# Optimization experiments

Measured on AMD Instinct MI355X. Metric: run time of the kernel, lower is better.

The kernel has to match this reference:

```python
import jax, jax.numpy as jnp
import numpy as np

N, C, H = 4096, 1024, 16
HD = C // H            # 64
DR = HD // 8           # 8 rope freqs per spatial axis


def setup_inputs() -> dict:
    key = jax.random.key(0)
    k1, k2, k3, k4, k5, k6 = jax.random.split(key, 6)
    x = jax.random.normal(k1, (N, C), dtype=jnp.float32)
    coords = jax.random.randint(k2, (N, 5), 0, 64, dtype=jnp.int32)  # [batch, t, h, w, z]
    w_qkv = jax.random.normal(k3, (3 * C, C), dtype=jnp.float32) / np.sqrt(C)
    w_out = jax.random.normal(k4, (C, C), dtype=jnp.float32) / np.sqrt(C)
    gamma_q = jnp.ones((H, HD), dtype=jnp.float32)
    gamma_k = jnp.ones((H, HD), dtype=jnp.float32)
    return {"x": x, "coords": coords, "w_qkv": w_qkv, "w_out": w_out,
            "gamma_q": gamma_q, "gamma_k": gamma_k}


def _rms_norm(t, gamma):
    # F.normalize(dim=-1) * gamma * sqrt(head_dim), computed in fp32
    t = t.astype(jnp.float32)
    nrm = jnp.linalg.norm(t, axis=-1, keepdims=True)
    return t / jnp.maximum(nrm, 1e-12) * gamma * np.float32(np.sqrt(HD))


def _rope_angles(coords):
    # freqs = 1/10000^(arange(DR)/HD); angles per axis (t,h,w,z), concat -> [N, 4*DR] = [N, HD/2]
    freqs = 1.0 / (10000.0 ** (jnp.arange(DR, dtype=jnp.float32) / HD))
    pos = coords[:, 1:].astype(jnp.float32)  # [N,4]
    ang = pos[:, :, None] * freqs[None, None, :]  # [N,4,DR]
    return ang.reshape(ang.shape[0], -1)  # [N, HD/2]


def _apply_rope(t, cos, sin):
    # t: [N,H,HD]; pairs (2i, 2i+1) rotated by angle[i]
    t2 = t.astype(jnp.float32).reshape(t.shape[0], t.shape[1], -1, 2)
    re = t2[..., 0] * cos - t2[..., 1] * sin
    im = t2[..., 0] * sin + t2[..., 1] * cos
    return jnp.stack([re, im], axis=-1).reshape(t.shape)


def reference(x, coords, w_qkv, w_out, gamma_q, gamma_k):
    n = x.shape[0]
    qkv = (x @ w_qkv.T).reshape(n, 3, H, HD)
    q, k, v = qkv[:, 0], qkv[:, 1], qkv[:, 2]  # [N,H,HD]
    q = _rms_norm(q, gamma_q)
    k = _rms_norm(k, gamma_k)
    ang = _rope_angles(coords)              # [N, HD/2]
    cos = jnp.cos(ang)[:, None, :]          # [N,1,HD/2] (broadcast over heads)
    sin = jnp.sin(ang)[:, None, :]
    q = _apply_rope(q, cos, sin)
    k = _apply_rope(k, cos, sin)
    scale = np.float32(1.0 / np.sqrt(HD))
    scores = jnp.einsum('nhd,mhd->hnm', q, k) * scale  # [H,N,N]
    attn = jax.nn.softmax(scores, axis=-1)
    out = jnp.einsum('hnm,mhd->nhd', attn, v).reshape(n, C)
    return out @ w_out.T
```

## Files before the change

kernel.cpp:

```cpp
#include <hip/hip_runtime.h>
#include <hip/hip_bf16.h>

typedef _Float16 half8 __attribute__((ext_vector_type(8)));
typedef _Float16 half4v __attribute__((ext_vector_type(4)));
typedef _Float16 half2 __attribute__((ext_vector_type(2)));
typedef float f32x4 __attribute__((ext_vector_type(4)));

constexpr int NT = 4096;
constexpr int CH = 1024;
constexpr int NH = 16;
constexpr int HD = 64;
constexpr int C3 = 3072;

#if __has_builtin(__builtin_amdgcn_exp2f)
#define EXP2(x) __builtin_amdgcn_exp2f(x)
#else
#define EXP2(x) exp2f(x)
#endif

#define GLOAD_LDS16(gp, lp) __builtin_amdgcn_global_load_lds( \
    (const __attribute__((address_space(1))) void*)(gp),      \
    (__attribute__((address_space(3))) void*)(lp), 16, 0, 0)

#define WAITCNT3 do { asm volatile("s_waitcnt vmcnt(3)" ::: "memory"); \
                      __builtin_amdgcn_sched_barrier(0); } while (0)
#define WAITCNT4 do { asm volatile("s_waitcnt vmcnt(4)" ::: "memory"); \
                      __builtin_amdgcn_sched_barrier(0); } while (0)
#define WAITCNT0 do { asm volatile("s_waitcnt vmcnt(0)" ::: "memory"); \
                      __builtin_amdgcn_sched_barrier(0); } while (0)

static __device__ inline half2 pk_f16(float a, float b) {
  auto r = __builtin_amdgcn_cvt_pkrtz(a, b);
  return *(half2*)&r;
}

__global__ __launch_bounds__(256) void cvt3_kernel(const float* __restrict__ a, int na4,
                                                   const float* __restrict__ b, int nb4,
                                                   const float* __restrict__ c, int nc4,
                                                   _Float16* __restrict__ oa,
                                                   _Float16* __restrict__ ob,
                                                   _Float16* __restrict__ oc) {
  int i = blockIdx.x * 256 + threadIdx.x;
  const float* src; _Float16* dst; int j = i;
  if (i < na4) { src = a; dst = oa; }
  else if (i < na4 + nb4) { src = b; dst = ob; j = i - na4; }
  else if (i < na4 + nb4 + nc4) { src = c; dst = oc; j = i - na4 - nb4; }
  else return;
  float4 v = ((const float4*)src)[j];
  half4v h;
  h[0] = (_Float16)v.x; h[1] = (_Float16)v.y; h[2] = (_Float16)v.z; h[3] = (_Float16)v.w;
  ((half4v*)dst)[j] = h;
}

__global__ __launch_bounds__(256) void rope_tab_kernel(const int* __restrict__ coords,
                                                       float2* __restrict__ csn) {
  int idx = blockIdx.x * 256 + threadIdx.x;
  int n = idx >> 5, j = idx & 31;
  float ang = (float)coords[n * 5 + 1 + (j >> 3)] * __expf(-(float)(j & 7) * 0.14391157f);
  csn[idx] = make_float2(cosf(ang), sinf(ang));
}

__global__ __launch_bounds__(512, 4) void gemm_qkv(const _Float16* __restrict__ A,
                                                   const _Float16* __restrict__ Bt,
                                                   const float2* __restrict__ csn,
                                                   const float* __restrict__ gq,
                                                   const float* __restrict__ gk,
                                                   _Float16* __restrict__ Qh,
                                                   _Float16* __restrict__ KF,
                                                   _Float16* __restrict__ VF) {
  __shared__ __align__(16) char smem[73728];
  auto As = (_Float16(*)[128][32])smem;
  auto Bs = (_Float16(*)[256][32])(smem + 16384);
  const int K = CH;
  const int tid = threadIdx.x;
  const int lane = tid & 63, w = tid >> 6;
  const int l15 = lane & 15, l4 = lane >> 4;
  int nwg = gridDim.x, cpx = nwg >> 3;
  int wg = (blockIdx.x & 7) * cpx + (blockIdx.x >> 3);
  const int nbx = NT / 128;
  const int bm = wg % nbx, bn = wg / nbx;
  const int m0 = bm * 128, n0 = bn * 256;
  const int wr = w >> 2, wc = w & 3;
  const int arow = w * 16 + (lane >> 2);
  const int acol = (lane & 3) * 8;
  const int rb = w * 32;
  const int rl = lane >> 2;
  const int cb = (lane & 3) * 8;
  f32x4 acc[4][4] = {};
  auto stage = [&](int k0, int buf) {
    GLOAD_LDS16(A  + (size_t)(m0 + arow) * K + k0 + acol,       &As[buf][w * 16][0]);
    GLOAD_LDS16(Bt + (size_t)(n0 + rb + rl) * K + k0 + cb,      &Bs[buf][rb][0]);
    GLOAD_LDS16(Bt + (size_t)(n0 + rb + 16 + rl) * K + k0 + cb, &Bs[buf][rb + 16][0]);
  };
  auto compute = [&](int buf) {
    half8 af[4], bf[4];
#pragma unroll
    for (int mt = 0; mt < 4; ++mt) af[mt] = *(half8*)&As[buf][wr * 64 + mt * 16 + l15][l4 * 8];
#pragma unroll
    for (int nt = 0; nt < 4; ++nt) bf[nt] = *(half8*)&Bs[buf][wc * 64 + nt * 16 + l15][l4 * 8];
    __builtin_amdgcn_s_setprio(1);
#pragma unroll
    for (int mt = 0; mt < 4; ++mt)
#pragma unroll
      for (int nt = 0; nt < 4; ++nt)
        acc[mt][nt] = __builtin_amdgcn_mfma_f32_16x16x32_f16(af[mt], bf[nt], acc[mt][nt], 0, 0, 0);
    __builtin_amdgcn_s_setprio(0);
  };
  stage(0, 0);
  stage(32, 1);
  for (int k0 = 0; k0 < K - 32; k0 += 32) {
    int buf = (k0 >> 5) & 1;
    WAITCNT3;
    __builtin_amdgcn_s_barrier();
    compute(buf);
    __builtin_amdgcn_s_barrier();
    if (k0 + 64 < K) stage(k0 + 64, buf);
  }
  WAITCNT0;
  __builtin_amdgcn_s_barrier();
  compute(((K - 32) >> 5) & 1);
  __builtin_amdgcn_s_barrier();
  const int gc0 = n0 + wc * 64;
  const int sec = gc0 >> 10;
  const int h   = (gc0 & 1023) >> 6;
  const int K0  = m0 + wr * 64;
  _Float16* Lw = (_Float16*)(smem + w * 9216);
  if (sec < 2) {
    const float* gm = (sec == 0) ? gq : gk;
    float gmm[4];
#pragma unroll
    for (int nt = 0; nt < 4; ++nt) gmm[nt] = gm[h * 64 + nt * 16 + l15];
    const float qsc = (sec == 0) ? 0.18033688f : 1.0f;
#pragma unroll
    for (int mt = 0; mt < 4; ++mt)
#pragma unroll
      for (int r = 0; r < 4; ++r) {
        float ss = 0.f;
#pragma unroll
        for (int nt = 0; nt < 4; ++nt) ss += acc[mt][nt][r] * acc[mt][nt][r];
        ss += __shfl_xor(ss, 1); ss += __shfl_xor(ss, 2);
        ss += __shfl_xor(ss, 4); ss += __shfl_xor(ss, 8);
        float sc = 8.0f / fmaxf(sqrtf(ss), 1e-12f);
        int row = mt * 16 + l4 * 4 + r;
        int n = K0 + row;
#pragma unroll
        for (int nt = 0; nt < 4; ++nt) {
          float v = acc[mt][nt][r] * sc * gmm[nt];
          float2 cz = csn[n * 32 + nt * 8 + (l15 >> 1)];
          float p = __shfl_xor(v, 1);
          float o = ((l15 & 1) == 0) ? (v * cz.x - p * cz.y) : (p * cz.y + v * cz.x);
          Lw[row * 72 + nt * 16 + l15] = (_Float16)(o * qsc);
        }
      }
  } else {
#pragma unroll
    for (int mt = 0; mt < 4; ++mt)
#pragma unroll
      for (int r = 0; r < 4; ++r) {
        int row = mt * 16 + l4 * 4 + r;
#pragma unroll
        for (int nt = 0; nt < 4; ++nt)
          Lw[row * 72 + nt * 16 + l15] = (_Float16)acc[mt][nt][r];
      }
  }
  const int kb = K0 >> 6;
  if (sec == 0) {
#pragma unroll
    for (int i = 0; i < 8; ++i) {
      int row = i * 8 + (lane >> 3), col = (lane & 7) * 8;
      half8 vv = *(half8*)&Lw[row * 72 + col];
      *(half8*)(Qh + ((size_t)h * NT + K0 + row) * 64 + col) = vv;
    }
  } else if (sec == 1) {
    _Float16* base = KF + (size_t)h * NT * HD + (size_t)kb * 4096;
#pragma unroll
    for (int i = 0; i < 8; ++i) {
      int t = i >> 1, kk = i & 1;
      int i15 = lane & 15, ll4 = lane >> 4;
      int m = ((t >> 1) << 5) | ((i15 >> 2) << 3) | ((t & 1) << 2) | (i15 & 3);
      half8 vv = *(half8*)&Lw[m * 72 + kk * 32 + ll4 * 8];
      *(half8*)(base + (size_t)(((t * 2 + kk) * 64 + ll4 * 16 + i15) * 8)) = vv;
    }
  } else {
    _Float16* base = VF + (size_t)h * NT * HD + (size_t)kb * 4096;
#pragma unroll
    for (int i = 0; i < 8; ++i) {
      int t = i >> 1, kk = i & 1;
      int l15v = lane & 15, l4v = lane >> 4;
      half8 vv;
#pragma unroll
      for (int jj = 0; jj < 8; ++jj)
        vv[jj] = Lw[(kk * 32 + l4v * 8 + jj) * 72 + t * 16 + l15v];
      *(half8*)(base + (size_t)(((t * 2 + kk) * 64 + l4v * 16 + l15v) * 8)) = vv;
    }
  }
}

template <typename OutT>
__global__ __launch_bounds__(256) void gemm_bt(const _Float16* __restrict__ A,
                                               const _Float16* __restrict__ Bt,
                                               OutT* __restrict__ Cc,
                                               int M, int Nn, int K, int nbx) {
  __shared__ _Float16 As[2][128][32];
  __shared__ _Float16 Bs[2][128][32];
  const int tid = threadIdx.x;
  const int lane = tid & 63, w = tid >> 6;
  const int l15 = lane & 15, l4 = lane >> 4;
  int nwg = gridDim.x, cpx = nwg >> 3;
  int wg = (blockIdx.x & 7) * cpx + (blockIdx.x >> 3);
  const int m0 = (wg % nbx) * 128, n0 = (wg / nbx) * 128;
  const int wr = w >> 1, wc = w & 1;
  const int rb = w * 32;
  const int rl = lane >> 2;
  const int cb = (lane & 3) * 8;
  f32x4 acc[4][4] = {};
  auto stage = [&](int k0, int buf) {
    GLOAD_LDS16(A  + (size_t)(m0 + rb + rl) * K + k0 + cb,      &As[buf][rb][0]);
    GLOAD_LDS16(A  + (size_t)(m0 + rb + 16 + rl) * K + k0 + cb, &As[buf][rb + 16][0]);
    GLOAD_LDS16(Bt + (size_t)(n0 + rb + rl) * K + k0 + cb,      &Bs[buf][rb][0]);
    GLOAD_LDS16(Bt + (size_t)(n0 + rb + 16 + rl) * K + k0 + cb, &Bs[buf][rb + 16][0]);
  };
  auto compute = [&](int buf) {
    half8 af[4], bf[4];
#pragma unroll
    for (int mt = 0; mt < 4; ++mt) af[mt] = *(half8*)&As[buf][wr * 64 + mt * 16 + l15][l4 * 8];
#pragma unroll
    for (int nt = 0; nt < 4; ++nt) bf[nt] = *(half8*)&Bs[buf][wc * 64 + nt * 16 + l15][l4 * 8];
    __builtin_amdgcn_s_setprio(1);
#pragma unroll
    for (int mt = 0; mt < 4; ++mt)
#pragma unroll
      for (int nt = 0; nt < 4; ++nt)
        acc[mt][nt] = __builtin_amdgcn_mfma_f32_16x16x32_f16(af[mt], bf[nt], acc[mt][nt], 0, 0, 0);
    __builtin_amdgcn_s_setprio(0);
  };
  stage(0, 0);
  stage(32, 1);
  for (int k0 = 0; k0 < K - 32; k0 += 32) {
    int buf = (k0 >> 5) & 1;
    WAITCNT4;
    __builtin_amdgcn_s_barrier();
    compute(buf);
    __builtin_amdgcn_s_barrier();
    if (k0 + 64 < K) stage(k0 + 64, buf);
  }
  WAITCNT0;
  __builtin_amdgcn_s_barrier();
  compute(((K - 32) >> 5) & 1);
#pragma unroll
  for (int mt = 0; mt < 4; ++mt)
#pragma unroll
    for (int nt = 0; nt < 4; ++nt)
#pragma unroll
      for (int r = 0; r < 4; ++r) {
        int row = m0 + wr * 64 + mt * 16 + l4 * 4 + r;
        int col = n0 + wc * 64 + nt * 16 + l15;
        Cc[(size_t)row * Nn + col] = (OutT)acc[mt][nt][r];
      }
}

__global__ __launch_bounds__(256, 2) void attn_kernel(const _Float16* __restrict__ Qh,
                                                      const _Float16* __restrict__ KF,
                                                      const _Float16* __restrict__ VF,
                                                      _Float16* __restrict__ Oh) {
  __shared__ _Float16 KB[4096];
  __shared__ _Float16 VB[4096];
  const int tid = threadIdx.x, lane = tid & 63, w = tid >> 6;
  const int l15 = lane & 15, l4 = lane >> 4;
  int bid = blockIdx.x;
  int s = bid >> 3;
  int h = (bid & 7) * 2 + (s >> 5);
  int n0 = (s & 31) * 128;
  half8 qf[2][2];
#pragma unroll
  for (int qb = 0; qb < 2; ++qb)
#pragma unroll
    for (int kk = 0; kk < 2; ++kk)
      qf[qb][kk] = *(const half8*)(Qh + ((size_t)h * NT + n0 + w * 32 + qb * 16 + l15) * HD + kk * 32 + l4 * 8);
  f32x4 acc[2][4] = {};
  f32x4 acc5[2] = {};
  half8 of1 = {};
  if (l15 == 0) {
#pragma unroll
    for (int jq = 0; jq < 8; ++jq) of1[jq] = (_Float16)1.0f;
  }
  const _Float16* KFh = KF + (size_t)h * NT * HD + w * 512 + lane * 8;
  const _Float16* VFh = VF + (size_t)h * NT * HD + w * 512 + lane * 8;
  union U { half8 v; half2 p[4]; };
  for (int kb = 0; kb < 64; ++kb) {
    __syncthreads();
    {
      size_t g0 = (size_t)kb * 4096;
      GLOAD_LDS16(KFh + g0,        &KB[w * 512]);
      GLOAD_LDS16(KFh + g0 + 2048, &KB[2048 + w * 512]);
      GLOAD_LDS16(VFh + g0,        &VB[w * 512]);
      GLOAD_LDS16(VFh + g0 + 2048, &VB[2048 + w * 512]);
    }
    __syncthreads();
    f32x4 sv[2][4] = {};
    __builtin_amdgcn_s_setprio(1);
#pragma unroll
    for (int t = 0; t < 4; ++t)
#pragma unroll
      for (int kk = 0; kk < 2; ++kk) {
        half8 kf = *(half8*)&KB[(t * 2 + kk) * 512 + lane * 8];
        sv[0][t] = __builtin_amdgcn_mfma_f32_16x16x32_f16(kf, qf[0][kk], sv[0][t], 0, 0, 0);
        sv[1][t] = __builtin_amdgcn_mfma_f32_16x16x32_f16(kf, qf[1][kk], sv[1][t], 0, 0, 0);
      }
    __builtin_amdgcn_s_setprio(0);
    U u[2][2];
#pragma unroll
    for (int qb = 0; qb < 2; ++qb) {
      float e[4][4];
#pragma unroll
      for (int t = 0; t < 4; ++t)
#pragma unroll
        for (int r = 0; r < 4; ++r) e[t][r] = EXP2(sv[qb][t][r]);
      u[qb][0].p[0] = pk_f16(e[0][0], e[0][1]); u[qb][0].p[1] = pk_f16(e[0][2], e[0][3]);
      u[qb][0].p[2] = pk_f16(e[1][0], e[1][1]); u[qb][0].p[3] = pk_f16(e[1][2], e[1][3]);
      u[qb][1].p[0] = pk_f16(e[2][0], e[2][1]); u[qb][1].p[1] = pk_f16(e[2][2], e[2][3]);
      u[qb][1].p[2] = pk_f16(e[3][0], e[3][1]); u[qb][1].p[3] = pk_f16(e[3][2], e[3][3]);
    }
    __builtin_amdgcn_s_setprio(1);
#pragma unroll
    for (int t = 0; t < 4; ++t)
#pragma unroll
      for (int kk = 0; kk < 2; ++kk) {
        half8 vf = *(half8*)&VB[(t * 2 + kk) * 512 + lane * 8];
        acc[0][t] = __builtin_amdgcn_mfma_f32_16x16x32_f16(u[0][kk].v, vf, acc[0][t], 0, 0, 0);
        acc[1][t] = __builtin_amdgcn_mfma_f32_16x16x32_f16(u[1][kk].v, vf, acc[1][t], 0, 0, 0);
      }
    acc5[0] = __builtin_amdgcn_mfma_f32_16x16x32_f16(u[0][0].v, of1, acc5[0], 0, 0, 0);
    acc5[0] = __builtin_amdgcn_mfma_f32_16x16x32_f16(u[0][1].v, of1, acc5[0], 0, 0, 0);
    acc5[1] = __builtin_amdgcn_mfma_f32_16x16x32_f16(u[1][0].v, of1, acc5[1], 0, 0, 0);
    acc5[1] = __builtin_amdgcn_mfma_f32_16x16x32_f16(u[1][1].v, of1, acc5[1], 0, 0, 0);
    __builtin_amdgcn_s_setprio(0);
  }
#pragma unroll
  for (int qb = 0; qb < 2; ++qb) {
    float linv[4];
#pragma unroll
    for (int r = 0; r < 4; ++r) linv[r] = 1.0f / __shfl(acc5[qb][r], lane & 48);
#pragma unroll
    for (int t = 0; t < 4; ++t)
#pragma unroll
      for (int r = 0; r < 4; ++r) {
        int row = n0 + w * 32 + qb * 16 + l4 * 4 + r;
        Oh[(size_t)row * CH + h * HD + t * 16 + l15] = (_Float16)(acc[qb][t][r] * linv[r]);
      }
  }
}

extern "C" void kernel_launch(void* const* d_in, const int* in_sizes, int n_in,
                              void* d_out, int out_size, void* d_ws, size_t ws_size,
                              hipStream_t stream) {
  const float* x      = (const float*)d_in[0];
  const int*   coords = (const int*)d_in[1];
  const float* w_qkv  = (const float*)d_in[2];
  const float* w_out  = (const float*)d_in[3];
  const float* gq     = (const float*)d_in[4];
  const float* gk     = (const float*)d_in[5];
  float* out = (float*)d_out;

  char* ws = (char*)d_ws;
  size_t off = 0;
  auto alloc = [&](size_t bytes) { char* p = ws + off; off += bytes; return p; };
  _Float16* xh   = (_Float16*)alloc((size_t)NT * CH * 2);
  _Float16* wqh  = (_Float16*)alloc((size_t)C3 * CH * 2);
  _Float16* woh  = (_Float16*)alloc((size_t)CH * CH * 2);
  float2*   csn  = (float2*)alloc((size_t)NT * 32 * 8);
  _Float16* Qh   = (_Float16*)alloc((size_t)NT * CH * 2);
  _Float16* KFh  = (_Float16*)alloc((size_t)NT * CH * 2);
  _Float16* VFh  = (_Float16*)alloc((size_t)NT * CH * 2);
  _Float16* Oh   = (_Float16*)alloc((size_t)NT * CH * 2);
  if (off > ws_size) return;

  int na4 = NT * CH / 4, nb4 = C3 * CH / 4, nc4 = CH * CH / 4;
  cvt3_kernel<<<(na4 + nb4 + nc4) / 256, 256, 0, stream>>>(x, na4, w_qkv, nb4, w_out, nc4,
                                                           xh, wqh, woh);
  rope_tab_kernel<<<NT * 32 / 256, 256, 0, stream>>>(coords, csn);
  gemm_qkv<<<(NT / 128) * (C3 / 256), 512, 0, stream>>>(xh, wqh, csn, gq, gk, Qh, KFh, VFh);
  attn_kernel<<<NH * (NT / 128), 256, 0, stream>>>(Qh, KFh, VFh, Oh);
  gemm_bt<float><<<(NT / 128) * (CH / 128), 256, 0, stream>>>(Oh, woh, out, NT, CH, CH, NT / 128);
}
```

Measured before the change: 154.4 us.

## Replace ones-MFMA row sums with VALU sums and load two KV tiles per barrier

The softmax denominator used to be computed with extra MFMAs against a ones vector. It is now accumulated in fp32 on the vector ALU from the exponentials and reduced across lanes with shuffles at the end. The main loop also fetches two 64-key K/V tiles per iteration into doubled LDS buffers, which halves the number of barrier pairs. This removes four MFMAs per tile and some synchronisation, at the cost of more VALU adds and more LDS use per block, which may lower occupancy.

```diff
diff --git a/kernel.cpp b/kernel.cpp
--- a/kernel.cpp
+++ b/kernel.cpp
@@ -263,8 +263,8 @@
                                                       const _Float16* __restrict__ KF,
                                                       const _Float16* __restrict__ VF,
                                                       _Float16* __restrict__ Oh) {
-  __shared__ _Float16 KB[4096];
-  __shared__ _Float16 VB[4096];
+  __shared__ _Float16 KB[2][4096];
+  __shared__ _Float16 VB[2][4096];
   const int tid = threadIdx.x, lane = tid & 63, w = tid >> 6;
   const int l15 = lane & 15, l4 = lane >> 4;
   int bid = blockIdx.x;
@@ -278,69 +278,77 @@
     for (int kk = 0; kk < 2; ++kk)
       qf[qb][kk] = *(const half8*)(Qh + ((size_t)h * NT + n0 + w * 32 + qb * 16 + l15) * HD + kk * 32 + l4 * 8);
   f32x4 acc[2][4] = {};
-  f32x4 acc5[2] = {};
-  half8 of1 = {};
-  if (l15 == 0) {
-#pragma unroll
-    for (int jq = 0; jq < 8; ++jq) of1[jq] = (_Float16)1.0f;
-  }
+  float ls[2] = {0.f, 0.f};
   const _Float16* KFh = KF + (size_t)h * NT * HD + w * 512 + lane * 8;
   const _Float16* VFh = VF + (size_t)h * NT * HD + w * 512 + lane * 8;
   union U { half8 v; half2 p[4]; };
-  for (int kb = 0; kb < 64; ++kb) {
+  for (int kb = 0; kb < 64; kb += 2) {
     __syncthreads();
     {
       size_t g0 = (size_t)kb * 4096;
-      GLOAD_LDS16(KFh + g0,        &KB[w * 512]);
-      GLOAD_LDS16(KFh + g0 + 2048, &KB[2048 + w * 512]);
-      GLOAD_LDS16(VFh + g0,        &VB[w * 512]);
-      GLOAD_LDS16(VFh + g0 + 2048, &VB[2048 + w * 512]);
+      GLOAD_LDS16(KFh + g0,        &KB[0][w * 512]);
+      GLOAD_LDS16(KFh + g0 + 2048, &KB[0][2048 + w * 512]);
+      GLOAD_LDS16(VFh + g0,        &VB[0][w * 512]);
+      GLOAD_LDS16(VFh + g0 + 2048, &VB[0][2048 + w * 512]);
+      GLOAD_LDS16(KFh + g0 + 4096, &KB[1][w * 512]);
+      GLOAD_LDS16(KFh + g0 + 6144, &KB[1][2048 + w * 512]);
+      GLOAD_LDS16(VFh + g0 + 4096, &VB[1][w * 512]);
+      GLOAD_LDS16(VFh + g0 + 6144, &VB[1][2048 + w * 512]);
     }
     __syncthreads();
-    f32x4 sv[2][4] = {};
-    __builtin_amdgcn_s_setprio(1);
-#pragma unroll
-    for (int t = 0; t < 4; ++t)
-#pragma unroll
-      for (int kk = 0; kk < 2; ++kk) {
-        half8 kf = *(half8*)&KB[(t * 2 + kk) * 512 + lane * 8];
-        sv[0][t] = __builtin_amdgcn_mfma_f32_16x16x32_f16(kf, qf[0][kk], sv[0][t], 0, 0, 0);
-        sv[1][t] = __builtin_amdgcn_mfma_f32_16x16x32_f16(kf, qf[1][kk], sv[1][t], 0, 0, 0);
-      }
-    __builtin_amdgcn_s_setprio(0);
-    U u[2][2];
-#pragma unroll
-    for (int qb = 0; qb < 2; ++qb) {
-      float e[4][4];
+#pragma unroll
+    for (int sub = 0; sub < 2; ++sub) {
+      f32x4 sv[2][4] = {};
+      __builtin_amdgcn_s_setprio(1);
 #pragma unroll
       for (int t = 0; t < 4; ++t)
 #pragma unroll
-        for (int r = 0; r < 4; ++r) e[t][r] = EXP2(sv[qb][t][r]);
-      u[qb][0].p[0] = pk_f16(e[0][0], e[0][1]); u[qb][0].p[1] = pk_f16(e[0][2], e[0][3]);
-      u[qb][0].p[2] = pk_f16(e[1][0], e[1][1]); u[qb][0].p[3] = pk_f16(e[1][2], e[1][3]);
-      u[qb][1].p[0] = pk_f16(e[2][0], e[2][1]); u[qb][1].p[1] = pk_f16(e[2][2], e[2][3]);
-      u[qb][1].p[2] = pk_f16(e[3][0], e[3][1]); u[qb][1].p[3] = pk_f16(e[3][2], e[3][3]);
-    }
-    __builtin_amdgcn_s_setprio(1);
-#pragma unroll
-    for (int t = 0; t < 4; ++t)
-#pragma unroll
-      for (int kk = 0; kk < 2; ++kk) {
-        half8 vf = *(half8*)&VB[(t * 2 + kk) * 512 + lane * 8];
-        acc[0][t] = __builtin_amdgcn_mfma_f32_16x16x32_f16(u[0][kk].v, vf, acc[0][t], 0, 0, 0);
-        acc[1][t] = __builtin_amdgcn_mfma_f32_16x16x32_f16(u[1][kk].v, vf, acc[1][t], 0, 0, 0);
-      }
-    acc5[0] = __builtin_amdgcn_mfma_f32_16x16x32_f16(u[0][0].v, of1, acc5[0], 0, 0, 0);
-    acc5[0] = __builtin_amdgcn_mfma_f32_16x16x32_f16(u[0][1].v, of1, acc5[0], 0, 0, 0);
-    acc5[1] = __builtin_amdgcn_mfma_f32_16x16x32_f16(u[1][0].v, of1, acc5[1], 0, 0, 0);
-    acc5[1] = __builtin_amdgcn_mfma_f32_16x16x32_f16(u[1][1].v, of1, acc5[1], 0, 0, 0);
-    __builtin_amdgcn_s_setprio(0);
+        for (int kk = 0; kk < 2; ++kk) {
+          half8 kf = *(half8*)&KB[sub][(t * 2 + kk) * 512 + lane * 8];
+          sv[0][t] = __builtin_amdgcn_mfma_f32_16x16x32_f16(kf, qf[0][kk], sv[0][t], 0, 0, 0);
+          sv[1][t] = __builtin_amdgcn_mfma_f32_16x16x32_f16(kf, qf[1][kk], sv[1][t], 0, 0, 0);
+        }
+      __builtin_amdgcn_s_setprio(0);
+      U u[2][2];
+#pragma unroll
+      for (int qb = 0; qb < 2; ++qb) {
+        float e[4][4];
+#pragma unroll
+        for (int t = 0; t < 4; ++t)
+#pragma unroll
+          for (int r = 0; r < 4; ++r) e[t][r] = EXP2(sv[qb][t][r]);
+        float s0 = (e[0][0] + e[0][1]) + (e[0][2] + e[0][3]);
+        float s1 = (e[1][0] + e[1][1]) + (e[1][2] + e[1][3]);
+        float s2 = (e[2][0] + e[2][1]) + (e[2][2] + e[2][3]);
+        float s3 = (e[3][0] + e[3][1]) + (e[3][2] + e[3][3]);
+        ls[qb] += (s0 + s1) + (s2 + s3);
+        u[qb][0].p[0] = pk_f16(e[0][0], e[0][1]); u[qb][0].p[1] = pk_f16(e[0][2], e[0][3]);
+        u[qb][0].p[2] = pk_f16(e[1][0], e[1][1]); u[qb][0].p[3] = pk_f16(e[1][2], e[1][3]);
+        u[qb][1].p[0] = pk_f16(e[2][0], e[2][1]); u[qb][1].p[1] = pk_f16(e[2][2], e[2][3]);
+        u[qb][1].p[2] = pk_f16(e[3][0], e[3][1]); u[qb][1].p[3] = pk_f16(e[3][2], e[3][3]);
+      }
+      __builtin_amdgcn_s_setprio(1);
+#pragma unroll
+      for (int t = 0; t < 4; ++t)
+#pragma unroll
+        for (int kk = 0; kk < 2; ++kk) {
+          half8 vf = *(half8*)&VB[sub][(t * 2 + kk) * 512 + lane * 8];
+          acc[0][t] = __builtin_amdgcn_mfma_f32_16x16x32_f16(u[0][kk].v, vf, acc[0][t], 0, 0, 0);
+          acc[1][t] = __builtin_amdgcn_mfma_f32_16x16x32_f16(u[1][kk].v, vf, acc[1][t], 0, 0, 0);
+        }
+      __builtin_amdgcn_s_setprio(0);
+    }
+  }
+#pragma unroll
+  for (int qb = 0; qb < 2; ++qb) {
+    ls[qb] += __shfl_xor(ls[qb], 16);
+    ls[qb] += __shfl_xor(ls[qb], 32);
   }
 #pragma unroll
   for (int qb = 0; qb < 2; ++qb) {
     float linv[4];
 #pragma unroll
-    for (int r = 0; r < 4; ++r) linv[r] = 1.0f / __shfl(acc5[qb][r], lane & 48);
+    for (int r = 0; r < 4; ++r) linv[r] = 1.0f / __shfl(ls[qb], l4 * 4 + r);
 #pragma unroll
     for (int t = 0; t < 4; ++t)
 #pragma unroll
```

Result: no change. 155.3 us (+0.6%).
